# Kernel tuning notes

Hardware: AMD Instinct MI355X
Metric: run time of the kernel (lower is better)

The kernel has to match this reference:

```python
import jax, jax.numpy as jnp
import numpy as np

S, B, D, H, F = 2048, 4, 1024, 16, 4096
DH = D // H  # per-head dim (nhid)
EPS = 1e-5


def layer_norm(x, g, b):
    m = jnp.mean(x, axis=-1, keepdims=True)
    v = jnp.mean((x - m) ** 2, axis=-1, keepdims=True)
    return (x - m) * jax.lax.rsqrt(v + EPS) * g + b


def setup_inputs() -> dict:
    key = jax.random.key(0)
    ks = jax.random.split(key, 16)
    s = 1.0 / np.sqrt(D)
    sf = 1.0 / np.sqrt(F)
    return {
        "x": jax.random.normal(ks[0], (S, B, D), dtype=jnp.float32),
        "ln1_g": jnp.ones((D,), jnp.float32),
        "ln1_b": jnp.zeros((D,), jnp.float32),
        "ln2_g": jnp.ones((D,), jnp.float32),
        "ln2_b": jnp.zeros((D,), jnp.float32),
        "Wq": jax.random.normal(ks[1], (D, D), jnp.float32) * s,
        "bq": jnp.zeros((D,), jnp.float32),
        "Wk": jax.random.normal(ks[2], (D, D), jnp.float32) * s,
        "bk": jnp.zeros((D,), jnp.float32),
        "Wv": jax.random.normal(ks[3], (D, D), jnp.float32) * s,
        "bv": jnp.zeros((D,), jnp.float32),
        "Wo": jax.random.normal(ks[4], (D, D), jnp.float32) * s,
        "bo": jnp.zeros((D,), jnp.float32),
        "W1": jax.random.normal(ks[5], (D, F), jnp.float32) * s,
        "b1": jnp.zeros((F,), jnp.float32),
        "W2": jax.random.normal(ks[6], (F, D), jnp.float32) * sf,
        "b2": jnp.zeros((D,), jnp.float32),
    }


def reference(x, ln1_g, ln1_b, ln2_g, ln2_b, Wq, bq, Wk, bk, Wv, bv, Wo, bo, W1, b1, W2, b2):
    # --- sublayer 0: LN -> full (non-causal) multi-head self-attention -> residual ---
    h = layer_norm(x, ln1_g, ln1_b)                      # [S,B,D]
    q = (h @ Wq + bq).reshape(S, B, H, DH)
    k = (h @ Wk + bk).reshape(S, B, H, DH)
    v = (h @ Wv + bv).reshape(S, B, H, DH)
    scale = 1.0 / jnp.sqrt(jnp.asarray(DH, x.dtype))
    scores = jnp.einsum("sbhd,tbhd->bhst", q, k) * scale  # [B,H,S,S]
    attn = jax.nn.softmax(scores, axis=-1)
    ctx = jnp.einsum("bhst,tbhd->sbhd", attn, v).reshape(S, B, D)
    x = x + (ctx @ Wo + bo)
    # --- sublayer 1: LN -> position-wise FFN -> residual ---
    h2 = layer_norm(x, ln2_g, ln2_b)
    ff = jax.nn.relu(h2 @ W1 + b1) @ W2 + b2
    return x + ff
```

## Files before the change

### kernel.cpp

```cpp
#include <hip/hip_runtime.h>
#include <hip/hip_bf16.h>
#include <stdint.h>

constexpr int S = 2048;
constexpr int B = 4;
constexpr int D = 1024;
constexpr int H = 16;
constexpr int F = 4096;
constexpr int DH = 64;
constexpr int N = S * B;

typedef __attribute__((ext_vector_type(8))) short  bf16x8;
typedef __attribute__((ext_vector_type(4))) float  floatx4;

__device__ __forceinline__ unsigned short f2bf(float f) {
    __hip_bfloat16 h = __float2bfloat16(f);
    return __builtin_bit_cast(unsigned short, h);
}
__device__ __forceinline__ uint32_t pack_bf2_fast(float a, float b) {
    uint32_t ua = __builtin_bit_cast(uint32_t, a) + 0x8000u;
    uint32_t ub = __builtin_bit_cast(uint32_t, b) + 0x8000u;
    return (ua >> 16) | (ub & 0xffff0000u);
}
__device__ __forceinline__ void glds16(const unsigned short* g, unsigned short* l) {
    __builtin_amdgcn_global_load_lds((__attribute__((address_space(1))) void*)(g),
                                     (__attribute__((address_space(3))) void*)(l),
                                     16, 0, 0);
}

__global__ __launch_bounds__(256) void convert_transpose(
    const float* __restrict__ src, unsigned short* __restrict__ dst, int K, int M) {
    __shared__ float tile[32][33];
    const int m0 = blockIdx.x * 32;
    const int k0 = blockIdx.y * 32;
    const int tx = threadIdx.x;
    const int ty = threadIdx.y;
    #pragma unroll
    for (int i = 0; i < 32; i += 8)
        tile[ty + i][tx] = src[(size_t)(k0 + ty + i) * M + m0 + tx];
    __syncthreads();
    #pragma unroll
    for (int i = 0; i < 32; i += 8)
        dst[(size_t)(m0 + ty + i) * K + k0 + tx] = f2bf(tile[tx][ty + i]);
}

__global__ __launch_bounds__(256) void transpose_v(
    const unsigned short* __restrict__ v, unsigned short* __restrict__ vt) {
    __shared__ unsigned short t[64][72];
    const int tid = threadIdx.x;
    const int s0 = blockIdx.x * 64;
    const int h  = blockIdx.y;
    const int b  = blockIdx.z;
    #pragma unroll
    for (int i = 0; i < 2; i++) {
        int c = i * 256 + tid;
        int row = c >> 3, off = (c & 7) * 8;
        *(uint4*)&t[row][off] =
            *(const uint4*)(v + ((size_t)(s0 + row) * B + b) * D + h * 64 + off);
    }
    __syncthreads();
    #pragma unroll
    for (int i = 0; i < 2; i++) {
        int c = i * 256 + tid;
        int dh = c >> 3, off = (c & 7) * 8;
        unsigned short tmp[8];
        #pragma unroll
        for (int j = 0; j < 8; j++) tmp[j] = t[off + j][dh];
        *(uint4*)(vt + ((size_t)((b * H + h) * 64 + dh)) * S + s0 + off) = *(uint4*)tmp;
    }
}

__global__ __launch_bounds__(256) void ln_kernel(
    const float* __restrict__ x, const float* __restrict__ g,
    const float* __restrict__ b, unsigned short* __restrict__ out) {
    const int row = blockIdx.x;
    const int tid = threadIdx.x;
    float4 v = ((const float4*)(x + (size_t)row * D))[tid];
    float s  = v.x + v.y + v.z + v.w;
    float ss = v.x * v.x + v.y * v.y + v.z * v.z + v.w * v.w;
    #pragma unroll
    for (int o = 32; o > 0; o >>= 1) {
        s  += __shfl_down(s,  o, 64);
        ss += __shfl_down(ss, o, 64);
    }
    __shared__ float red[8];
    __shared__ float mv[2];
    const int wv = tid >> 6, ln = tid & 63;
    if (ln == 0) { red[wv] = s; red[4 + wv] = ss; }
    __syncthreads();
    if (tid == 0) {
        float S2 = red[0] + red[1] + red[2] + red[3];
        float SS = red[4] + red[5] + red[6] + red[7];
        float mean = S2 * (1.0f / D);
        float var  = SS * (1.0f / D) - mean * mean;
        mv[0] = mean;
        mv[1] = rsqrtf(var + 1e-5f);
    }
    __syncthreads();
    const float mean = mv[0], inv = mv[1];
    float4 gv = ((const float4*)g)[tid];
    float4 bv = ((const float4*)b)[tid];
    ushort4 o4;
    o4.x = f2bf((v.x - mean) * inv * gv.x + bv.x);
    o4.y = f2bf((v.y - mean) * inv * gv.y + bv.y);
    o4.z = f2bf((v.z - mean) * inv * gv.z + bv.z);
    o4.w = f2bf((v.w - mean) * inv * gv.w + bv.w);
    ((ushort4*)(out + (size_t)row * D))[tid] = o4;
}

template <int RELU, int RESID, int OUT_BF16>
__global__ __launch_bounds__(256, 2) void gemm_bt(
    const unsigned short* __restrict__ A,
    const unsigned short* __restrict__ Bt,
    const float* __restrict__ bias,
    const float* __restrict__ resid,
    void* __restrict__ out,
    int M, int K) {
    __shared__ __align__(16) unsigned short As[128 * 32];
    __shared__ __align__(16) unsigned short Bs[128 * 32];

    const int tid  = threadIdx.x;
    const int lane = tid & 63;
    const int wave = tid >> 6;
    const int wr = (wave >> 1) * 64;
    const int wc = (wave & 1) * 64;
    const int n0 = blockIdx.y * 128;
    const int m0 = blockIdx.x * 128;
    const int quad = lane >> 4;
    const int r    = lane & 15;

    floatx4 acc[4][4] = {};

    const int l4 = lane >> 2;
    const int lc = lane & 3;
    const int seg0 = 2 * wave, seg1 = 2 * wave + 1;
    const int rowA0 = seg0 * 16 + l4;
    const int rowA1 = seg1 * 16 + l4;
    const int kch0 = ((lc ^ ((rowA0 >> 1) & 3)) * 8);
    const int kch1 = ((lc ^ ((rowA1 >> 1) & 3)) * 8);
    const unsigned short* gA0 = A  + (size_t)(n0 + rowA0) * K + kch0;
    const unsigned short* gA1 = A  + (size_t)(n0 + rowA1) * K + kch1;
    const unsigned short* gB0 = Bt + (size_t)(m0 + rowA0) * K + kch0;
    const unsigned short* gB1 = Bt + (size_t)(m0 + rowA1) * K + kch1;
    unsigned short* lA0 = As + seg0 * 512;
    unsigned short* lA1 = As + seg1 * 512;
    unsigned short* lB0 = Bs + seg0 * 512;
    unsigned short* lB1 = Bs + seg1 * 512;

    const int fc = (quad ^ ((r >> 1) & 3)) * 8;

    for (int k0 = 0; k0 < K; k0 += 32) {
        __syncthreads();
        glds16(gA0, lA0);
        glds16(gA1, lA1);
        glds16(gB0, lB0);
        glds16(gB1, lB1);
        gA0 += 32; gA1 += 32; gB0 += 32; gB1 += 32;
        __syncthreads();

        bf16x8 af[4], bfr[4];
        #pragma unroll
        for (int i = 0; i < 4; i++)
            af[i] = *(const bf16x8*)&As[(wr + i * 16 + r) * 32 + fc];
        #pragma unroll
        for (int j = 0; j < 4; j++)
            bfr[j] = *(const bf16x8*)&Bs[(wc + j * 16 + r) * 32 + fc];
        #pragma unroll
        for (int i = 0; i < 4; i++)
            #pragma unroll
            for (int j = 0; j < 4; j++)
                acc[i][j] = __builtin_amdgcn_mfma_f32_16x16x32_bf16(af[i], bfr[j], acc[i][j], 0, 0, 0);
    }

    #pragma unroll
    for (int i = 0; i < 4; i++) {
        #pragma unroll
        for (int j = 0; j < 4; j++) {
            const int row = n0 + wr + i * 16 + quad * 4;
            const int col = m0 + wc + j * 16 + r;
            const float bcol = bias[col];
            #pragma unroll
            for (int rr = 0; rr < 4; rr++) {
                float val = acc[i][j][rr] + bcol;
                if constexpr (RESID) val += resid[(size_t)(row + rr) * M + col];
                if constexpr (RELU)  val = fmaxf(val, 0.0f);
                if constexpr (OUT_BF16)
                    ((unsigned short*)out)[(size_t)(row + rr) * M + col] = f2bf(val);
                else
                    ((float*)out)[(size_t)(row + rr) * M + col] = val;
            }
        }
    }
}

__global__ __launch_bounds__(256, 3) void flash_attn(
    const unsigned short* __restrict__ q,
    const unsigned short* __restrict__ k,
    const unsigned short* __restrict__ vt,
    unsigned short* __restrict__ ctx) {
    constexpr int LQK = 72;
    constexpr int LP  = 136;
    constexpr float SCL = 0.18033688011112042f;

    __shared__ __align__(16) unsigned short Ks[128 * LQK];
    __shared__ __align__(16) unsigned short Ps[128 * LP];

    const int tid  = threadIdx.x;
    const int lane = tid & 63;
    const int wave = tid >> 6;
    const int quad = lane >> 4;
    const int r    = lane & 15;
    const int s0 = blockIdx.x * 128;
    const int h  = blockIdx.y;
    const int b  = blockIdx.z;
    const int wq0 = wave * 32;

    unsigned short* Qs = Ks;
    #pragma unroll
    for (int i = 0; i < 4; i++) {
        int c = i * 256 + tid;
        int row = c >> 3, off = (c & 7) * 8;
        *(uint4*)&Qs[row * LQK + off] =
            *(const uint4*)(q + ((size_t)(s0 + row) * B + b) * D + h * 64 + off);
    }
    __syncthreads();
    bf16x8 qf[2][2];
    #pragma unroll
    for (int j = 0; j < 2; j++)
        #pragma unroll
        for (int kk = 0; kk < 2; kk++)
            qf[j][kk] = *(const bf16x8*)&Qs[(wq0 + j * 16 + r) * LQK + kk * 32 + quad * 8];

    const bf16x8 ones = {(short)0x3F80, (short)0x3F80, (short)0x3F80, (short)0x3F80,
                         (short)0x3F80, (short)0x3F80, (short)0x3F80, (short)0x3F80};

    uint4 kr[4];
    const unsigned short* kbase  = k  + (size_t)b * D + h * 64;
    const unsigned short* vtbase = vt + (size_t)((b * H + h) * 64) * S;
    #pragma unroll
    for (int i = 0; i < 4; i++) {
        int c = i * 256 + tid;
        int row = c >> 3, off = (c & 7) * 8;
        kr[i] = *(const uint4*)(kbase + (size_t)row * B * D + off);
    }

    floatx4 acc2[2][4] = {};
    floatx4 accD[2]    = {};

    for (int t = 0; t < S / 128; t++) {
        __syncthreads();
        #pragma unroll
        for (int i = 0; i < 4; i++) {
            int c = i * 256 + tid;
            int row = c >> 3, off = (c & 7) * 8;
            *(uint4*)&Ks[row * LQK + off] = kr[i];
        }
        __syncthreads();

        if (t + 1 < S / 128) {
            const size_t tb = (size_t)(t + 1) * 128;
            #pragma unroll
            for (int i = 0; i < 4; i++) {
                int c = i * 256 + tid;
                int row = c >> 3, off = (c & 7) * 8;
                kr[i] = *(const uint4*)(kbase + (tb + row) * B * D + off);
            }
        }

        const unsigned short* vrow = vtbase + (size_t)r * S + t * 128 + quad * 8;
        uint4 vbuf[2][4];
        #pragma unroll
        for (int ss = 0; ss < 2; ss++)
            #pragma unroll
            for (int jn = 0; jn < 4; jn++)
                vbuf[ss][jn] = *(const uint4*)(vrow + (size_t)(jn * 16) * S + ss * 32);

        #pragma unroll
        for (int i = 0; i < 8; i++) {
            bf16x8 kf0 = *(const bf16x8*)&Ks[(i * 16 + r) * LQK + quad * 8];
            bf16x8 kf1 = *(const bf16x8*)&Ks[(i * 16 + r) * LQK + 32 + quad * 8];
            #pragma unroll
            for (int j = 0; j < 2; j++) {
                floatx4 sc = {};
                sc = __builtin_amdgcn_mfma_f32_16x16x32_bf16(kf0, qf[j][0], sc, 0, 0, 0);
                sc = __builtin_amdgcn_mfma_f32_16x16x32_bf16(kf1, qf[j][1], sc, 0, 0, 0);
                float p0 = exp2f(sc[0] * SCL);
                float p1 = exp2f(sc[1] * SCL);
                float p2 = exp2f(sc[2] * SCL);
                float p3 = exp2f(sc[3] * SCL);
                uint2 w;
                w.x = pack_bf2_fast(p0, p1);
                w.y = pack_bf2_fast(p2, p3);
                *(uint2*)&Ps[(wq0 + j * 16 + r) * LP + i * 16 + quad * 4] = w;
            }
        }

        #pragma unroll
        for (int s = 0; s < 4; s++) {
            bf16x8 a2[2];
            #pragma unroll
            for (int j = 0; j < 2; j++)
                a2[j] = *(const bf16x8*)&Ps[(wq0 + j * 16 + r) * LP + s * 32 + quad * 8];
            bf16x8 b2[4];
            #pragma unroll
            for (int jn = 0; jn < 4; jn++)
                b2[jn] = __builtin_bit_cast(bf16x8, vbuf[s & 1][jn]);
            if (s < 2) {
                #pragma unroll
                for (int jn = 0; jn < 4; jn++)
                    vbuf[s & 1][jn] = *(const uint4*)(vrow + (size_t)(jn * 16) * S + (s + 2) * 32);
            }
            #pragma unroll
            for (int j = 0; j < 2; j++) {
                #pragma unroll
                for (int jn = 0; jn < 4; jn++)
                    acc2[j][jn] = __builtin_amdgcn_mfma_f32_16x16x32_bf16(a2[j], b2[jn], acc2[j][jn], 0, 0, 0);
                accD[j] = __builtin_amdgcn_mfma_f32_16x16x32_bf16(a2[j], ones, accD[j], 0, 0, 0);
            }
        }
    }

    float inv[2][4];
    #pragma unroll
    for (int j = 0; j < 2; j++)
        #pragma unroll
        for (int rr = 0; rr < 4; rr++)
            inv[j][rr] = 1.0f / accD[j][rr];

    #pragma unroll
    for (int j = 0; j < 2; j++) {
        #pragma unroll
        for (int jn = 0; jn < 4; jn++) {
            #pragma unroll
            for (int rr = 0; rr < 4; rr++) {
                const int qrow = wq0 + j * 16 + quad * 4 + rr;
                const int dh   = jn * 16 + r;
                const float val = acc2[j][jn][rr] * inv[j][rr];
                ctx[((size_t)(s0 + qrow) * B + b) * D + h * 64 + dh] = f2bf(val);
            }
        }
    }
}

extern "C" void kernel_launch(void* const* d_in, const int* in_sizes, int n_in,
                              void* d_out, int out_size, void* d_ws, size_t ws_size,
                              hipStream_t stream) {
    const float* x    = (const float*)d_in[0];
    const float* ln1g = (const float*)d_in[1];
    const float* ln1b = (const float*)d_in[2];
    const float* ln2g = (const float*)d_in[3];
    const float* ln2b = (const float*)d_in[4];
    const float* Wq   = (const float*)d_in[5];
    const float* bq   = (const float*)d_in[6];
    const float* Wk   = (const float*)d_in[7];
    const float* bk   = (const float*)d_in[8];
    const float* Wv   = (const float*)d_in[9];
    const float* bv   = (const float*)d_in[10];
    const float* Wo   = (const float*)d_in[11];
    const float* bo   = (const float*)d_in[12];
    const float* W1   = (const float*)d_in[13];
    const float* b1   = (const float*)d_in[14];
    const float* W2   = (const float*)d_in[15];
    const float* b2   = (const float*)d_in[16];
    float* out = (float*)d_out;

    char* ws = (char*)d_ws;
    const size_t MB = 1ull << 20;
    unsigned short* wqT = (unsigned short*)(ws + 0 * MB);
    unsigned short* wkT = (unsigned short*)(ws + 2 * MB);
    unsigned short* wvT = (unsigned short*)(ws + 4 * MB);
    unsigned short* woT = (unsigned short*)(ws + 6 * MB);
    unsigned short* w1T = (unsigned short*)(ws + 8 * MB);
    unsigned short* w2T = (unsigned short*)(ws + 16 * MB);
    unsigned short* h   = (unsigned short*)(ws + 24 * MB);
    unsigned short* qb  = (unsigned short*)(ws + 40 * MB);
    unsigned short* kb  = (unsigned short*)(ws + 56 * MB);
    unsigned short* vb  = (unsigned short*)(ws + 72 * MB);
    unsigned short* ctx = (unsigned short*)(ws + 88 * MB);
    float*          x1  = (float*)(ws + 104 * MB);
    unsigned short* vt  = (unsigned short*)(ws + 104 * MB);
    unsigned short* ff1 = qb;
    unsigned short* h2  = h;

    const dim3 tb(32, 8);
    convert_transpose<<<dim3(D / 32, D / 32), tb, 0, stream>>>(Wq, wqT, D, D);
    convert_transpose<<<dim3(D / 32, D / 32), tb, 0, stream>>>(Wk, wkT, D, D);
    convert_transpose<<<dim3(D / 32, D / 32), tb, 0, stream>>>(Wv, wvT, D, D);
    convert_transpose<<<dim3(D / 32, D / 32), tb, 0, stream>>>(Wo, woT, D, D);
    convert_transpose<<<dim3(F / 32, D / 32), tb, 0, stream>>>(W1, w1T, D, F);
    convert_transpose<<<dim3(D / 32, F / 32), tb, 0, stream>>>(W2, w2T, F, D);

    ln_kernel<<<N, 256, 0, stream>>>(x, ln1g, ln1b, h);

    const dim3 g1(D / 128, N / 128);
    gemm_bt<0, 0, 1><<<g1, 256, 0, stream>>>(h, wqT, bq, nullptr, qb, D, D);
    gemm_bt<0, 0, 1><<<g1, 256, 0, stream>>>(h, wkT, bk, nullptr, kb, D, D);
    gemm_bt<0, 0, 1><<<g1, 256, 0, stream>>>(h, wvT, bv, nullptr, vb, D, D);

    transpose_v<<<dim3(S / 64, H, B), 256, 0, stream>>>(vb, vt);

    flash_attn<<<dim3(S / 128, H, B), 256, 0, stream>>>(qb, kb, vt, ctx);

    gemm_bt<0, 1, 0><<<g1, 256, 0, stream>>>(ctx, woT, bo, x, x1, D, D);

    ln_kernel<<<N, 256, 0, stream>>>(x1, ln2g, ln2b, h2);

    gemm_bt<1, 0, 1><<<dim3(F / 128, N / 128), 256, 0, stream>>>(h2, w1T, b1, nullptr, ff1, F, D);

    gemm_bt<0, 1, 0><<<g1, 256, 0, stream>>>(ff1, w2T, b2, x1, out, D, F);
}
```

Baseline: 666.6 us.

## Fuse QKV GEMMs, deepen GEMM K-tile, remap attention blocks for XCD locality

The three Q/K/V projections become one GEMM against a concatenated transposed weight and bias, writing an interleaved QKV buffer that the V transpose and attention read with new strides. The GEMM K-step doubles to 64 with a new XOR swizzle, and occupancy is raised to 3 blocks per CU. Flash attention now uses a flat grid that groups each (batch, head) on one XCD to improve L2 reuse of K/V. The V tile for the whole step is prefetched into registers up front. The aim is fewer launches and syncs per K and better cache locality, at the cost of more registers and LDS per block.

```diff
diff --git a/kernel.cpp b/kernel.cpp
--- a/kernel.cpp
+++ b/kernel.cpp
@@ -9,6 +9,7 @@
 constexpr int F = 4096;
 constexpr int DH = 64;
 constexpr int N = S * B;
+constexpr int QKVS = 3 * D;
 
 typedef __attribute__((ext_vector_type(8))) short  bf16x8;
 typedef __attribute__((ext_vector_type(4))) float  floatx4;
@@ -44,8 +45,16 @@
         dst[(size_t)(m0 + ty + i) * K + k0 + tx] = f2bf(tile[tx][ty + i]);
 }
 
+__global__ __launch_bounds__(256) void concat_bias(
+    const float* __restrict__ bq, const float* __restrict__ bk,
+    const float* __restrict__ bv, float* __restrict__ dst) {
+    int i = blockIdx.x * 256 + threadIdx.x;
+    float v = (i < 1024) ? bq[i] : (i < 2048 ? bk[i - 1024] : bv[i - 2048]);
+    dst[i] = v;
+}
+
 __global__ __launch_bounds__(256) void transpose_v(
-    const unsigned short* __restrict__ v, unsigned short* __restrict__ vt) {
+    const unsigned short* __restrict__ qkv, unsigned short* __restrict__ vt) {
     __shared__ unsigned short t[64][72];
     const int tid = threadIdx.x;
     const int s0 = blockIdx.x * 64;
@@ -56,7 +65,7 @@
         int c = i * 256 + tid;
         int row = c >> 3, off = (c & 7) * 8;
         *(uint4*)&t[row][off] =
-            *(const uint4*)(v + ((size_t)(s0 + row) * B + b) * D + h * 64 + off);
+            *(const uint4*)(qkv + ((size_t)(s0 + row) * B + b) * QKVS + 2048 + h * 64 + off);
     }
     __syncthreads();
     #pragma unroll
@@ -109,15 +118,15 @@
 }
 
 template <int RELU, int RESID, int OUT_BF16>
-__global__ __launch_bounds__(256, 2) void gemm_bt(
+__global__ __launch_bounds__(256, 3) void gemm_bt(
     const unsigned short* __restrict__ A,
     const unsigned short* __restrict__ Bt,
     const float* __restrict__ bias,
     const float* __restrict__ resid,
     void* __restrict__ out,
     int M, int K) {
-    __shared__ __align__(16) unsigned short As[128 * 32];
-    __shared__ __align__(16) unsigned short Bs[128 * 32];
+    __shared__ __align__(16) unsigned short As[128 * 64];
+    __shared__ __align__(16) unsigned short Bs[128 * 64];
 
     const int tid  = threadIdx.x;
     const int lane = tid & 63;
@@ -131,45 +140,39 @@
 
     floatx4 acc[4][4] = {};
 
-    const int l4 = lane >> 2;
-    const int lc = lane & 3;
-    const int seg0 = 2 * wave, seg1 = 2 * wave + 1;
-    const int rowA0 = seg0 * 16 + l4;
-    const int rowA1 = seg1 * 16 + l4;
-    const int kch0 = ((lc ^ ((rowA0 >> 1) & 3)) * 8);
-    const int kch1 = ((lc ^ ((rowA1 >> 1) & 3)) * 8);
-    const unsigned short* gA0 = A  + (size_t)(n0 + rowA0) * K + kch0;
-    const unsigned short* gA1 = A  + (size_t)(n0 + rowA1) * K + kch1;
-    const unsigned short* gB0 = Bt + (size_t)(m0 + rowA0) * K + kch0;
-    const unsigned short* gB1 = Bt + (size_t)(m0 + rowA1) * K + kch1;
-    unsigned short* lA0 = As + seg0 * 512;
-    unsigned short* lA1 = As + seg1 * 512;
-    unsigned short* lB0 = Bs + seg0 * 512;
-    unsigned short* lB1 = Bs + seg1 * 512;
-
-    const int fc = (quad ^ ((r >> 1) & 3)) * 8;
-
-    for (int k0 = 0; k0 < K; k0 += 32) {
+    const int l8  = lane >> 3;
+    const int gch = ((lane & 7) ^ l8) * 8;
+    const unsigned short* gA = A  + (size_t)(n0 + wave * 32 + l8) * K + gch;
+    const unsigned short* gB = Bt + (size_t)(m0 + wave * 32 + l8) * K + gch;
+    unsigned short* lA = As + wave * 32 * 64;
+    unsigned short* lB = Bs + wave * 32 * 64;
+    const size_t rowstep = (size_t)8 * K;
+
+    for (int k0 = 0; k0 < K; k0 += 64) {
         __syncthreads();
-        glds16(gA0, lA0);
-        glds16(gA1, lA1);
-        glds16(gB0, lB0);
-        glds16(gB1, lB1);
-        gA0 += 32; gA1 += 32; gB0 += 32; gB1 += 32;
+        #pragma unroll
+        for (int c = 0; c < 4; c++) glds16(gA + c * rowstep, lA + c * 512);
+        #pragma unroll
+        for (int c = 0; c < 4; c++) glds16(gB + c * rowstep, lB + c * 512);
+        gA += 64; gB += 64;
         __syncthreads();
 
-        bf16x8 af[4], bfr[4];
-        #pragma unroll
-        for (int i = 0; i < 4; i++)
-            af[i] = *(const bf16x8*)&As[(wr + i * 16 + r) * 32 + fc];
-        #pragma unroll
-        for (int j = 0; j < 4; j++)
-            bfr[j] = *(const bf16x8*)&Bs[(wc + j * 16 + r) * 32 + fc];
-        #pragma unroll
-        for (int i = 0; i < 4; i++)
+        #pragma unroll
+        for (int kk = 0; kk < 2; kk++) {
+            const int fc = ((kk * 4 + quad) ^ (r & 7)) * 8;
+            bf16x8 af[4], bfr[4];
+            #pragma unroll
+            for (int i = 0; i < 4; i++)
+                af[i] = *(const bf16x8*)&As[(wr + i * 16 + r) * 64 + fc];
             #pragma unroll
             for (int j = 0; j < 4; j++)
-                acc[i][j] = __builtin_amdgcn_mfma_f32_16x16x32_bf16(af[i], bfr[j], acc[i][j], 0, 0, 0);
+                bfr[j] = *(const bf16x8*)&Bs[(wc + j * 16 + r) * 64 + fc];
+            #pragma unroll
+            for (int i = 0; i < 4; i++)
+                #pragma unroll
+                for (int j = 0; j < 4; j++)
+                    acc[i][j] = __builtin_amdgcn_mfma_f32_16x16x32_bf16(af[i], bfr[j], acc[i][j], 0, 0, 0);
+        }
     }
 
     #pragma unroll
@@ -194,8 +197,7 @@
 }
 
 __global__ __launch_bounds__(256, 3) void flash_attn(
-    const unsigned short* __restrict__ q,
-    const unsigned short* __restrict__ k,
+    const unsigned short* __restrict__ qkv,
     const unsigned short* __restrict__ vt,
     unsigned short* __restrict__ ctx) {
     constexpr int LQK = 72;
@@ -210,10 +212,14 @@
     const int wave = tid >> 6;
     const int quad = lane >> 4;
     const int r    = lane & 15;
-    const int s0 = blockIdx.x * 128;
-    const int h  = blockIdx.y;
-    const int b  = blockIdx.z;
-    const int wq0 = wave * 32;
+    const int flat = blockIdx.x;
+    const int xcd  = flat & 7;
+    const int t0   = (flat >> 3) & 15;
+    const int bh   = (flat >> 7) * 8 + xcd;
+    const int b    = bh >> 4;
+    const int h    = bh & 15;
+    const int s0   = t0 * 128;
+    const int wq0  = wave * 32;
 
     unsigned short* Qs = Ks;
     #pragma unroll
@@ -221,7 +227,7 @@
         int c = i * 256 + tid;
         int row = c >> 3, off = (c & 7) * 8;
         *(uint4*)&Qs[row * LQK + off] =
-            *(const uint4*)(q + ((size_t)(s0 + row) * B + b) * D + h * 64 + off);
+            *(const uint4*)(qkv + ((size_t)(s0 + row) * B + b) * QKVS + h * 64 + off);
     }
     __syncthreads();
     bf16x8 qf[2][2];
@@ -235,13 +241,13 @@
                          (short)0x3F80, (short)0x3F80, (short)0x3F80, (short)0x3F80};
 
     uint4 kr[4];
-    const unsigned short* kbase  = k  + (size_t)b * D + h * 64;
+    const unsigned short* kbase  = qkv + (size_t)b * QKVS + 1024 + h * 64;
     const unsigned short* vtbase = vt + (size_t)((b * H + h) * 64) * S;
     #pragma unroll
     for (int i = 0; i < 4; i++) {
         int c = i * 256 + tid;
         int row = c >> 3, off = (c & 7) * 8;
-        kr[i] = *(const uint4*)(kbase + (size_t)row * B * D + off);
+        kr[i] = *(const uint4*)(kbase + (size_t)row * B * QKVS + off);
     }
 
     floatx4 acc2[2][4] = {};
@@ -257,23 +263,23 @@
         }
         __syncthreads();
 
+        const unsigned short* vrow = vtbase + (size_t)r * S + t * 128 + quad * 8;
+        uint4 vbuf[4][4];
+        #pragma unroll
+        for (int ss = 0; ss < 4; ss++)
+            #pragma unroll
+            for (int jn = 0; jn < 4; jn++)
+                vbuf[ss][jn] = *(const uint4*)(vrow + (size_t)(jn * 16) * S + ss * 32);
+
         if (t + 1 < S / 128) {
             const size_t tb = (size_t)(t + 1) * 128;
             #pragma unroll
             for (int i = 0; i < 4; i++) {
                 int c = i * 256 + tid;
                 int row = c >> 3, off = (c & 7) * 8;
-                kr[i] = *(const uint4*)(kbase + (tb + row) * B * D + off);
+                kr[i] = *(const uint4*)(kbase + (tb + row) * B * QKVS + off);
             }
         }
-
-        const unsigned short* vrow = vtbase + (size_t)r * S + t * 128 + quad * 8;
-        uint4 vbuf[2][4];
-        #pragma unroll
-        for (int ss = 0; ss < 2; ss++)
-            #pragma unroll
-            for (int jn = 0; jn < 4; jn++)
-                vbuf[ss][jn] = *(const uint4*)(vrow + (size_t)(jn * 16) * S + ss * 32);
 
         #pragma unroll
         for (int i = 0; i < 8; i++) {
@@ -301,20 +307,12 @@
             #pragma unroll
             for (int j = 0; j < 2; j++)
                 a2[j] = *(const bf16x8*)&Ps[(wq0 + j * 16 + r) * LP + s * 32 + quad * 8];
-            bf16x8 b2[4];
-            #pragma unroll
-            for (int jn = 0; jn < 4; jn++)
-                b2[jn] = __builtin_bit_cast(bf16x8, vbuf[s & 1][jn]);
-            if (s < 2) {
-                #pragma unroll
-                for (int jn = 0; jn < 4; jn++)
-                    vbuf[s & 1][jn] = *(const uint4*)(vrow + (size_t)(jn * 16) * S + (s + 2) * 32);
-            }
             #pragma unroll
             for (int j = 0; j < 2; j++) {
                 #pragma unroll
                 for (int jn = 0; jn < 4; jn++)
-                    acc2[j][jn] = __builtin_amdgcn_mfma_f32_16x16x32_bf16(a2[j], b2[jn], acc2[j][jn], 0, 0, 0);
+                    acc2[j][jn] = __builtin_amdgcn_mfma_f32_16x16x32_bf16(
+                        a2[j], __builtin_bit_cast(bf16x8, vbuf[s][jn]), acc2[j][jn], 0, 0, 0);
                 accD[j] = __builtin_amdgcn_mfma_f32_16x16x32_bf16(a2[j], ones, accD[j], 0, 0, 0);
             }
         }
@@ -335,8 +333,8 @@
             for (int rr = 0; rr < 4; rr++) {
                 const int qrow = wq0 + j * 16 + quad * 4 + rr;
                 const int dh   = jn * 16 + r;
-                const float val = acc2[j][jn][rr] * inv[j][rr];
-                ctx[((size_t)(s0 + qrow) * B + b) * D + h * 64 + dh] = f2bf(val);
+                ctx[((size_t)(s0 + qrow) * B + b) * D + h * 64 + dh] =
+                    f2bf(acc2[j][jn][rr] * inv[j][rr]);
             }
         }
     }
@@ -366,41 +364,38 @@
 
     char* ws = (char*)d_ws;
     const size_t MB = 1ull << 20;
-    unsigned short* wqT = (unsigned short*)(ws + 0 * MB);
-    unsigned short* wkT = (unsigned short*)(ws + 2 * MB);
-    unsigned short* wvT = (unsigned short*)(ws + 4 * MB);
-    unsigned short* woT = (unsigned short*)(ws + 6 * MB);
-    unsigned short* w1T = (unsigned short*)(ws + 8 * MB);
-    unsigned short* w2T = (unsigned short*)(ws + 16 * MB);
-    unsigned short* h   = (unsigned short*)(ws + 24 * MB);
-    unsigned short* qb  = (unsigned short*)(ws + 40 * MB);
-    unsigned short* kb  = (unsigned short*)(ws + 56 * MB);
-    unsigned short* vb  = (unsigned short*)(ws + 72 * MB);
-    unsigned short* ctx = (unsigned short*)(ws + 88 * MB);
-    float*          x1  = (float*)(ws + 104 * MB);
-    unsigned short* vt  = (unsigned short*)(ws + 104 * MB);
-    unsigned short* ff1 = qb;
-    unsigned short* h2  = h;
+    unsigned short* wqkvT = (unsigned short*)(ws + 0 * MB);
+    unsigned short* woT   = (unsigned short*)(ws + 6 * MB);
+    unsigned short* w1T   = (unsigned short*)(ws + 8 * MB);
+    unsigned short* w2T   = (unsigned short*)(ws + 16 * MB);
+    unsigned short* h     = (unsigned short*)(ws + 24 * MB);
+    unsigned short* qkv   = (unsigned short*)(ws + 40 * MB);
+    unsigned short* ctx   = (unsigned short*)(ws + 88 * MB);
+    float*          bqkv  = (float*)(ws + 88 * MB);
+    float*          x1    = (float*)(ws + 104 * MB);
+    unsigned short* vt    = (unsigned short*)(ws + 104 * MB);
+    unsigned short* ff1   = qkv;
+    unsigned short* h2    = h;
 
     const dim3 tb(32, 8);
-    convert_transpose<<<dim3(D / 32, D / 32), tb, 0, stream>>>(Wq, wqT, D, D);
-    convert_transpose<<<dim3(D / 32, D / 32), tb, 0, stream>>>(Wk, wkT, D, D);
-    convert_transpose<<<dim3(D / 32, D / 32), tb, 0, stream>>>(Wv, wvT, D, D);
+    convert_transpose<<<dim3(D / 32, D / 32), tb, 0, stream>>>(Wq, wqkvT, D, D);
+    convert_transpose<<<dim3(D / 32, D / 32), tb, 0, stream>>>(Wk, wqkvT + (size_t)D * D, D, D);
+    convert_transpose<<<dim3(D / 32, D / 32), tb, 0, stream>>>(Wv, wqkvT + 2 * (size_t)D * D, D, D);
     convert_transpose<<<dim3(D / 32, D / 32), tb, 0, stream>>>(Wo, woT, D, D);
     convert_transpose<<<dim3(F / 32, D / 32), tb, 0, stream>>>(W1, w1T, D, F);
     convert_transpose<<<dim3(D / 32, F / 32), tb, 0, stream>>>(W2, w2T, F, D);
+    concat_bias<<<12, 256, 0, stream>>>(bq, bk, bv, bqkv);
 
     ln_kernel<<<N, 256, 0, stream>>>(x, ln1g, ln1b, h);
 
+    gemm_bt<0, 0, 1><<<dim3(3 * D / 128, N / 128), 256, 0, stream>>>(
+        h, wqkvT, bqkv, nullptr, qkv, 3 * D, D);
+
+    transpose_v<<<dim3(S / 64, H, B), 256, 0, stream>>>(qkv, vt);
+
+    flash_attn<<<dim3((S / 128) * H * B), 256, 0, stream>>>(qkv, vt, ctx);
+
     const dim3 g1(D / 128, N / 128);
-    gemm_bt<0, 0, 1><<<g1, 256, 0, stream>>>(h, wqT, bq, nullptr, qb, D, D);
-    gemm_bt<0, 0, 1><<<g1, 256, 0, stream>>>(h, wkT, bk, nullptr, kb, D, D);
-    gemm_bt<0, 0, 1><<<g1, 256, 0, stream>>>(h, wvT, bv, nullptr, vb, D, D);
-
-    transpose_v<<<dim3(S / 64, H, B), 256, 0, stream>>>(vb, vt);
-
-    flash_attn<<<dim3(S / 128, H, B), 256, 0, stream>>>(qb, kb, vt, ctx);
-
     gemm_bt<0, 1, 0><<<g1, 256, 0, stream>>>(ctx, woT, bo, x, x1, D, D);
 
     ln_kernel<<<N, 256, 0, stream>>>(x1, ln2g, ln2b, h2);
```

Measured after the change: 722.5 us. 1.08x slower.
